# Kernel tuning notes

Hardware: AMD Instinct MI355X
Metric: run time of the kernel (lower is better)

The kernel has to match this reference:

```python
import jax, jax.numpy as jnp
import numpy as np

# Irreps structure (hardcoded per init_kwargs):
#  input  = 16x0e + 8x1o  -> dim 16 + 8*3 = 40
#  query  = key = 8x0e + 4x1o -> dim 8 + 4*3 = 20
#  output = 16x0e + 8x1o -> dim 40
#  edge_sh = 1x0e + 1x1o -> dim 4
M0, M1 = 16, 8          # input multiplicities (scalar, vector)
Q0, Q1 = 8, 4           # query/key multiplicities
O0, O1 = 16, 8          # output multiplicities
TPK_NUMEL = M0*Q0 + M1*Q0 + M0*Q1 + M1*Q1 + M1*Q1   # 320
TPV_NUMEL = M0*O0 + M1*O0 + M0*O1 + M1*O1 + M1*O1   # 640
EDGE_BASIS = 16
HIDDEN = 32


def _split(x):
    """Split irreps vector [*, m0 + 3*m1] into scalars [*, m0] and vectors [*, m1, 3]."""
    m0 = x.shape[-1] - 3 * ((x.shape[-1] - M0) // 3) if False else None
    return x  # placeholder, not used


def fc_net(x, w1, w2):
    """e3nn FullyConnectedNet: no biases, 1/sqrt(fan_in) scaling, silu hidden act."""
    h = jax.nn.silu((x @ w1) * (1.0 / np.sqrt(x.shape[-1])))
    return (h @ w2) * (1.0 / np.sqrt(w1.shape[-1]))


def fctp_edge(xs, xv, shs, shv, w, o0, o1):
    """FullyConnectedTensorProduct((m0x0e+m1x1o) x (1x0e+1x1o) -> (o0x0e+o1x1o))
    with per-edge weights w [E, numel]. Component-normalized CG, path-normalized output.
    xs:[E,m0] xv:[E,m1,3] shs:[E,1] shv:[E,3]."""
    m0, m1 = xs.shape[1], xv.shape[1]
    sizes = [m0*o0, m1*o0, m0*o1, m1*o1, m1*o1]
    offs = np.cumsum([0] + sizes)
    w1 = w[:, offs[0]:offs[1]].reshape(-1, m0, o0)
    w2 = w[:, offs[1]:offs[2]].reshape(-1, m1, o0)
    w3 = w[:, offs[2]:offs[3]].reshape(-1, m0, o1)
    w4 = w[:, offs[3]:offs[4]].reshape(-1, m1, o1)
    w5 = w[:, offs[4]:offs[5]].reshape(-1, m1, o1)
    # scalar output paths: 0e x 0e -> 0e ; 1o x 1o -> 0e (dot / sqrt3)
    p_ss = xs * shs                                            # [E,m0]
    p_vv = jnp.einsum('eic,ec->ei', xv, shv) * (1.0/np.sqrt(3.0))  # [E,m1]
    out_s = (jnp.einsum('ei,eio->eo', p_ss, w1)
             + jnp.einsum('ei,eio->eo', p_vv, w2)) * (1.0/np.sqrt(m0 + m1))
    # vector output paths: 0e x 1o ; 1o x 0e ; 1o x 1o -> 1o (cross / sqrt2)
    p_sv = xs[:, :, None] * shv[:, None, :]                    # [E,m0,3]
    p_vs = xv * shs[:, :, None]                                # [E,m1,3]
    p_xx = jnp.cross(xv, shv[:, None, :]) * (1.0/np.sqrt(2.0)) # [E,m1,3]
    out_v = (jnp.einsum('eic,eio->eoc', p_sv, w3)
             + jnp.einsum('eic,eio->eoc', p_vs, w4)
             + jnp.einsum('eic,eio->eoc', p_xx, w5)) * (1.0/np.sqrt(m0 + 2*m1))
    return out_s, out_v


def setup_inputs() -> dict:
    key = jax.random.key(0)
    ks = jax.random.split(key, 12)
    N, E = 10000, 100000
    node_ft = jax.random.normal(ks[0], (N, M0 + 3*M1), dtype=jnp.float32)
    edge_index = jax.random.randint(ks[1], (2, E), 0, N, dtype=jnp.int64)
    edge_sh = jax.random.normal(ks[2], (E, 4), dtype=jnp.float32)
    edge_scalars = jax.random.uniform(ks[3], (E, EDGE_BASIS), dtype=jnp.float32)
    # learned parameters
    w_q_s = jax.random.normal(ks[4], (M0, Q0), dtype=jnp.float32)
    w_q_v = jax.random.normal(ks[5], (M1, Q1), dtype=jnp.float32)
    fck_w1 = jax.random.normal(ks[6], (EDGE_BASIS, HIDDEN), dtype=jnp.float32)
    fck_w2 = jax.random.normal(ks[7], (HIDDEN, TPK_NUMEL), dtype=jnp.float32)
    fcv_w1 = jax.random.normal(ks[8], (EDGE_BASIS, HIDDEN), dtype=jnp.float32)
    fcv_w2 = jax.random.normal(ks[9], (HIDDEN, TPV_NUMEL), dtype=jnp.float32)
    wdot_s = jax.random.normal(ks[10], (Q0, Q0), dtype=jnp.float32)
    wdot_v = jax.random.normal(ks[11], (Q1, Q1), dtype=jnp.float32)
    return dict(node_ft=node_ft, edge_index=edge_index, edge_sh=edge_sh,
                edge_scalars=edge_scalars, w_q_s=w_q_s, w_q_v=w_q_v,
                fck_w1=fck_w1, fck_w2=fck_w2, fcv_w1=fcv_w1, fcv_w2=fcv_w2,
                wdot_s=wdot_s, wdot_v=wdot_v)


def reference(node_ft, edge_index, edge_sh, edge_scalars, w_q_s, w_q_v,
              fck_w1, fck_w2, fcv_w1, fcv_w2, wdot_s, wdot_v):
    N = node_ft.shape[0]
    sender, receiver = edge_index[0], edge_index[1]
    x_s = node_ft[:, :M0]                       # [N,16]
    x_v = node_ft[:, M0:].reshape(N, M1, 3)     # [N,8,3]
    # q = o3.Linear(input -> query): per-irrep linear mixing, 1/sqrt(mul) norm
    q_s = (x_s @ w_q_s) * (1.0/np.sqrt(M0))                    # [N,Q0]
    q_v = jnp.einsum('nic,io->noc', x_v, w_q_v) * (1.0/np.sqrt(M1))  # [N,Q1,3]
    sh_s, sh_v = edge_sh[:, :1], edge_sh[:, 1:4]
    xs_e, xv_e = x_s[sender], x_v[sender]       # gather sender features
    # per-edge tensor-product weights from radial MLPs
    wk = fc_net(edge_scalars, fck_w1, fck_w2)   # [E, 320]
    wv = fc_net(edge_scalars, fcv_w1, fcv_w2)   # [E, 640]
    k_s, k_v = fctp_edge(xs_e, xv_e, sh_s, sh_v, wk, Q0, Q1)
    v_s, v_v = fctp_edge(xs_e, xv_e, sh_s, sh_v, wv, O0, O1)
    # dot = FCTP(query, key -> 0e) with shared internal weights
    qr_s, qr_v = q_s[receiver], q_v[receiver]
    fan = Q0*Q0 + Q1*Q1
    dot = (jnp.einsum('ei,ej,ij->e', qr_s, k_s, wdot_s)
           + jnp.einsum('eic,ejc,ij->e', qr_v, k_v, wdot_v) * (1.0/np.sqrt(3.0))
           ) * (1.0/np.sqrt(fan))               # [E]
    # scatter-softmax over receiver
    ex = jnp.exp(dot)
    z = jax.ops.segment_sum(ex, receiver, num_segments=N)      # [N]
    alpha = ex / z[receiver]
    a = jnp.sqrt(jax.nn.relu(alpha))            # [E]
    out_s = jax.ops.segment_sum(a[:, None] * v_s, receiver, num_segments=N)
    out_v = jax.ops.segment_sum(a[:, None, None] * v_v, receiver, num_segments=N)
    return jnp.concatenate([out_s, out_v.reshape(N, O1*3)], axis=-1)  # [N,40]
```

## Files before the change

### kernel.cpp

```cpp
#include <hip/hip_runtime.h>


#define BS 256
#define EPB 64

typedef _Float16 h2 __attribute__((ext_vector_type(2)));

__device__ __forceinline__ float silu_f(float x) {
    return x * (1.0f / (1.0f + __expf(-x)));
}
__device__ __forceinline__ unsigned short f2h(float f) {
    return __builtin_bit_cast(unsigned short, (_Float16)f);
}
__device__ __forceinline__ unsigned pk2h(float a, float b) {
    return (unsigned)f2h(a) | ((unsigned)f2h(b) << 16);
}
__device__ __forceinline__ h2 uh2(unsigned u) {
    return __builtin_bit_cast(h2, u);
}
__device__ __forceinline__ h2 pkrtz(float a, float b) {
    return __builtin_bit_cast(h2, __builtin_amdgcn_cvt_pkrtz(a, b));
}
__device__ __forceinline__ h2 pfma(h2 a, h2 b, h2 c) {
    return __builtin_elementwise_fma(a, b, c);
}
__device__ __forceinline__ float h2s(h2 a) {
    return (float)a[0] + (float)a[1];
}
__device__ __forceinline__ float wred4(float v) {
    v += __shfl_xor(v, 16);
    v += __shfl_xor(v, 32);
    return v;
}

__global__ __launch_bounds__(256) void pre_count(
    const float* __restrict__ node_ft,
    const int*   __restrict__ ei,
    const float* __restrict__ w_q_s, const float* __restrict__ w_q_v,
    const float* __restrict__ wdot_s, const float* __restrict__ wdot_v,
    float* __restrict__ qd, int* __restrict__ cnt, int* __restrict__ flag,
    int N, int E)
{
    const int gid = blockIdx.x * blockDim.x + threadIdx.x;

    int acc = 0;
    if ((threadIdx.x & 63) == 0) {
        const int kmax = (E < 64) ? E : 64;
        for (int k = 0; k < kmax; ++k) acc |= ei[2*k + 1];
    }
    acc = __shfl(acc, 0, 64);
    const int is64 = (acc == 0) ? 1 : 0;
    if (gid == 0) *flag = is64;

    if (gid < E) {
        const int rcv = is64 ? ei[2*(E + gid)] : ei[E + gid];
        atomicAdd(cnt + rcv, 1);
    }

    const int n = gid;
    if (n >= N) return;

    const float* nf = node_ft + (size_t)n * 40;
    float xs[16];
#pragma unroll
    for (int i = 0; i < 16; ++i) xs[i] = nf[i];
    float qv0[8];
#pragma unroll
    for (int o = 0; o < 8; ++o) {
        float a = 0.f;
#pragma unroll
        for (int i = 0; i < 16; ++i) a += xs[i] * w_q_s[i*8 + o];
        qv0[o] = a * 0.25f;
    }
    float* qdn = qd + (size_t)n * 20;
#pragma unroll
    for (int j = 0; j < 8; ++j) {
        float a = 0.f;
#pragma unroll
        for (int i = 0; i < 8; ++i) a += qv0[i] * wdot_s[i*8 + j];
        qdn[j] = a;
    }
    float xv[8][3];
#pragma unroll
    for (int i = 0; i < 8; ++i)
#pragma unroll
        for (int c = 0; c < 3; ++c) xv[i][c] = nf[16 + i*3 + c];
    float qv[4][3];
#pragma unroll
    for (int o = 0; o < 4; ++o)
#pragma unroll
        for (int c = 0; c < 3; ++c) {
            float a = 0.f;
#pragma unroll
            for (int i = 0; i < 8; ++i) a += xv[i][c] * w_q_v[i*4 + o];
            qv[o][c] = a * 0.35355339059327379f;
        }
#pragma unroll
    for (int j = 0; j < 4; ++j)
#pragma unroll
        for (int c = 0; c < 3; ++c) {
            float a = 0.f;
#pragma unroll
            for (int i = 0; i < 4; ++i) a += qv[i][c] * wdot_v[i*4 + j];
            qdn[8 + j*3 + c] = a;
        }
}

__global__ __launch_bounds__(1024) void scan_kernel(
    const int* __restrict__ cnt, int* __restrict__ start,
    int* __restrict__ cursor, int N)
{
    __shared__ int wsum[16];
    __shared__ int s_carry;
    const int tid = threadIdx.x, wave = tid >> 6, lane = tid & 63;
    if (tid == 0) s_carry = 0;
    __syncthreads();
    for (int base = 0; base < N; base += 1024) {
        const int i = base + tid;
        const int v = (i < N) ? cnt[i] : 0;
        int x = v;
#pragma unroll
        for (int d = 1; d < 64; d <<= 1) {
            const int y = __shfl_up(x, d, 64);
            if (lane >= d) x += y;
        }
        if (lane == 63) wsum[wave] = x;
        __syncthreads();
        if (wave == 0 && lane < 16) {
            int w = wsum[lane];
#pragma unroll
            for (int d = 1; d < 16; d <<= 1) {
                const int y = __shfl_up(w, d, 64);
                if (lane >= d) w += y;
            }
            wsum[lane] = w;
        }
        __syncthreads();
        const int woff = (wave == 0) ? 0 : wsum[wave - 1];
        const int carry = s_carry;
        if (i < N) {
            const int s = carry + woff + x - v;
            start[i] = s;
            cursor[i] = s;
        }
        __syncthreads();
        if (tid == 0) s_carry = carry + wsum[15];
        __syncthreads();
    }
    if (tid == 0) start[N] = s_carry;
}

__global__ __launch_bounds__(BS) void edge_all(
    const float* __restrict__ node_ft,
    const int*   __restrict__ ei,
    const float* __restrict__ edge_sh,
    const float* __restrict__ edge_scalars,
    const float* __restrict__ fck_w1,
    const float* __restrict__ fck_w2,
    const float* __restrict__ fcv_w1,
    const float* __restrict__ fcv_w2,
    const float* __restrict__ qd,
    int*   __restrict__ cursor,
    float* __restrict__ exbuf,
    float* __restrict__ vbuf,
    const int* __restrict__ flag,
    int N, int E)
{
    __shared__ uint4 swz[4 * 385];

    const int tid = threadIdx.x;
    const int lane = tid & 63;
    const int p = lane >> 4;
    const int q = lane & 15;
    const int w = tid >> 6;
    const int e = blockIdx.x * EPB + w * 16 + q;
    const bool val = (e < E);
    const int ec = val ? e : (E - 1);

    const int is64 = *flag;
    const int snd = is64 ? ei[2*ec]       : ei[ec];
    const int rcv = is64 ? ei[2*(E + ec)] : ei[E + ec];

    int pos = 0;
    if (p == 0 && val) pos = atomicAdd(cursor + rcv, 1);

    const float4 s4 = *(const float4*)(edge_sh + (size_t)ec * 4);
    const float sh_s = s4.x;
    const float sh_v[3] = {s4.y, s4.z, s4.w};
    const float* nf = node_ft + (size_t)snd * 40;
    const float c3 = 0.57735026918962576f;
    const float c7 = 0.70710678118654752f;

    float es[16];
    {
        const float4* a0 = (const float4*)(edge_scalars + (size_t)ec * 16);
#pragma unroll
        for (int t = 0; t < 4; ++t) {
            const float4 v = a0[t];
            es[4*t+0]=v.x; es[4*t+1]=v.y; es[4*t+2]=v.z; es[4*t+3]=v.w;
        }
    }

    for (int idx = tid; idx < 4 * 320; idx += BS) {
        const int pg = idx / 320;
        const int local = idx - pg * 320;
        unsigned r0, r1, r2, r3;
        if (local < 128) {
            const int j = local >> 2, rr = local & 3, ip = rr >> 1, h = rr & 1;
            const int i0 = 4*pg + 2*ip;
            const float* s0 = fck_w2 + j*320 + i0*8 + 4*h;
            const float* s1 = s0 + 8;
            r0 = pk2h(s0[0], s1[0]); r1 = pk2h(s0[1], s1[1]);
            r2 = pk2h(s0[2], s1[2]); r3 = pk2h(s0[3], s1[3]);
        } else if (local < 192) {
            const int l = local - 128; const int j = l >> 1, ip = l & 1;
            const int i0 = 4*pg + 2*ip;
            const float* s0 = fck_w2 + j*320 + 192 + i0*4;
            const float* s1 = s0 + 4;
            r0 = pk2h(s0[0], s1[0]); r1 = pk2h(s0[1], s1[1]);
            r2 = pk2h(s0[2], s1[2]); r3 = pk2h(s0[3], s1[3]);
        } else if (local < 256) {
            const int l = local - 192; const int j = l >> 1, h = l & 1;
            const int i0 = 2*pg;
            const float* s0 = fck_w2 + j*320 + 128 + i0*8 + 4*h;
            const float* s1 = s0 + 8;
            r0 = pk2h(s0[0], s1[0]); r1 = pk2h(s0[1], s1[1]);
            r2 = pk2h(s0[2], s1[2]); r3 = pk2h(s0[3], s1[3]);
        } else {
            const int l = local - 256; const int jp = l >> 2, rr = l & 3;
            const int il = rr >> 1, h = rr & 1;
            const int i = 2*pg + il, j0 = 2*jp;
            const int col = (h == 0 ? 256 : 288) + i*4;
            const float* s0 = fck_w2 + j0*320 + col;
            const float* s1 = s0 + 320;
            r0 = pk2h(s0[0], s1[0]); r1 = pk2h(s0[1], s1[1]);
            r2 = pk2h(s0[2], s1[2]); r3 = pk2h(s0[3], s1[3]);
        }
        swz[pg * 321 + local] = make_uint4(r0, r1, r2, r3);
    }
    __syncthreads();

    float sa = 0.f;
    {
        float hk[32];
#pragma unroll
        for (int j = 0; j < 32; ++j) {
            float a = 0.f;
#pragma unroll
            for (int t = 0; t < 16; ++t) a += es[t] * fck_w1[t*32 + j];
            hk[j] = silu_f(a * 0.25f);
        }

        const uint4* g = swz + p * 321;

        const h2 xs01 = pkrtz(nf[4*p + 0], nf[4*p + 1]);
        const h2 xs23 = pkrtz(nf[4*p + 2], nf[4*p + 3]);
        const float x00 = nf[16 + 6*p], x01 = nf[17 + 6*p], x02 = nf[18 + 6*p];
        const float x10 = nf[19 + 6*p], x11 = nf[20 + 6*p], x12 = nf[21 + 6*p];
        const h2 pvp = pkrtz((x00*sh_v[0] + x01*sh_v[1] + x02*sh_v[2]) * c3,
                             (x10*sh_v[0] + x11*sh_v[1] + x12*sh_v[2]) * c3);

        h2 K1[8] = {}, K3[4] = {}, K2[8] = {};
#pragma unroll
        for (int j = 0; j < 32; ++j) {
            const uint4 A = g[j*4+0], B = g[j*4+1], C = g[j*4+2], D = g[j*4+3];
            const uint4 Ea = g[128 + j*2], Fb = g[128 + j*2 + 1];
            const uint4 U = g[192 + j*2], V = g[192 + j*2 + 1];
            const h2 hh = pkrtz(hk[j], hk[j]);
            const h2 t01 = hh * xs01, t23 = hh * xs23, tp = hh * pvp;
            K1[0]=pfma(t01,uh2(A.x),K1[0]); K1[0]=pfma(t23,uh2(C.x),K1[0]);
            K1[1]=pfma(t01,uh2(A.y),K1[1]); K1[1]=pfma(t23,uh2(C.y),K1[1]);
            K1[2]=pfma(t01,uh2(A.z),K1[2]); K1[2]=pfma(t23,uh2(C.z),K1[2]);
            K1[3]=pfma(t01,uh2(A.w),K1[3]); K1[3]=pfma(t23,uh2(C.w),K1[3]);
            K1[4]=pfma(t01,uh2(B.x),K1[4]); K1[4]=pfma(t23,uh2(D.x),K1[4]);
            K1[5]=pfma(t01,uh2(B.y),K1[5]); K1[5]=pfma(t23,uh2(D.y),K1[5]);
            K1[6]=pfma(t01,uh2(B.z),K1[6]); K1[6]=pfma(t23,uh2(D.z),K1[6]);
            K1[7]=pfma(t01,uh2(B.w),K1[7]); K1[7]=pfma(t23,uh2(D.w),K1[7]);
            K3[0]=pfma(t01,uh2(Ea.x),K3[0]); K3[0]=pfma(t23,uh2(Fb.x),K3[0]);
            K3[1]=pfma(t01,uh2(Ea.y),K3[1]); K3[1]=pfma(t23,uh2(Fb.y),K3[1]);
            K3[2]=pfma(t01,uh2(Ea.z),K3[2]); K3[2]=pfma(t23,uh2(Fb.z),K3[2]);
            K3[3]=pfma(t01,uh2(Ea.w),K3[3]); K3[3]=pfma(t23,uh2(Fb.w),K3[3]);
            K2[0]=pfma(tp,uh2(U.x),K2[0]); K2[1]=pfma(tp,uh2(U.y),K2[1]);
            K2[2]=pfma(tp,uh2(U.z),K2[2]); K2[3]=pfma(tp,uh2(U.w),K2[3]);
            K2[4]=pfma(tp,uh2(V.x),K2[4]); K2[5]=pfma(tp,uh2(V.y),K2[5]);
            K2[6]=pfma(tp,uh2(V.z),K2[6]); K2[7]=pfma(tp,uh2(V.w),K2[7]);
        }

        h2 P4[8] = {}, P5[8] = {};
#pragma unroll
        for (int jp = 0; jp < 16; ++jp) {
            const uint4 a4 = g[256 + jp*4 + 0];
            const uint4 b4 = g[256 + jp*4 + 1];
            const uint4 c4 = g[256 + jp*4 + 2];
            const uint4 d4 = g[256 + jp*4 + 3];
            const h2 hp = pkrtz(hk[2*jp], hk[2*jp+1]);
            P4[0]=pfma(hp,uh2(a4.x),P4[0]); P4[1]=pfma(hp,uh2(a4.y),P4[1]);
            P4[2]=pfma(hp,uh2(a4.z),P4[2]); P4[3]=pfma(hp,uh2(a4.w),P4[3]);
            P5[0]=pfma(hp,uh2(b4.x),P5[0]); P5[1]=pfma(hp,uh2(b4.y),P5[1]);
            P5[2]=pfma(hp,uh2(b4.z),P5[2]); P5[3]=pfma(hp,uh2(b4.w),P5[3]);
            P4[4]=pfma(hp,uh2(c4.x),P4[4]); P4[5]=pfma(hp,uh2(c4.y),P4[5]);
            P4[6]=pfma(hp,uh2(c4.z),P4[6]); P4[7]=pfma(hp,uh2(c4.w),P4[7]);
            P5[4]=pfma(hp,uh2(d4.x),P5[4]); P5[5]=pfma(hp,uh2(d4.y),P5[5]);
            P5[6]=pfma(hp,uh2(d4.z),P5[6]); P5[7]=pfma(hp,uh2(d4.w),P5[7]);
        }

        float ds = 0.f, dv = 0.f;
        {
            float qdr[20];
            const float4* rp = (const float4*)(qd + (size_t)rcv * 20);
#pragma unroll
            for (int t = 0; t < 5; ++t) {
                const float4 a = rp[t];
                qdr[4*t+0]=a.x; qdr[4*t+1]=a.y; qdr[4*t+2]=a.z; qdr[4*t+3]=a.w;
            }
#pragma unroll
            for (int o = 0; o < 8; ++o)
                ds += qdr[o] * (sh_s*h2s(K1[o]) + h2s(K2[o]));
            float KV[12] = {};
            {
                const float s0=sh_s*x00, s1=sh_s*x01, s2=sh_s*x02;
                const float cx0=c7*(x01*sh_v[2]-x02*sh_v[1]);
                const float cx1=c7*(x02*sh_v[0]-x00*sh_v[2]);
                const float cx2=c7*(x00*sh_v[1]-x01*sh_v[0]);
#pragma unroll
                for (int o = 0; o < 4; ++o) {
                    const float w4 = h2s(P4[o]), w5 = h2s(P5[o]);
                    KV[o*3+0] += s0*w4 + cx0*w5;
                    KV[o*3+1] += s1*w4 + cx1*w5;
                    KV[o*3+2] += s2*w4 + cx2*w5;
                }
            }
            {
                const float s0=sh_s*x10, s1=sh_s*x11, s2=sh_s*x12;
                const float cx0=c7*(x11*sh_v[2]-x12*sh_v[1]);
                const float cx1=c7*(x12*sh_v[0]-x10*sh_v[2]);
                const float cx2=c7*(x10*sh_v[1]-x11*sh_v[0]);
#pragma unroll
                for (int o = 0; o < 4; ++o) {
                    const float w4 = h2s(P4[4+o]), w5 = h2s(P5[4+o]);
                    KV[o*3+0] += s0*w4 + cx0*w5;
                    KV[o*3+1] += s1*w4 + cx1*w5;
                    KV[o*3+2] += s2*w4 + cx2*w5;
                }
            }
#pragma unroll
            for (int o = 0; o < 4; ++o) {
                const float k3 = h2s(K3[o]);
#pragma unroll
                for (int c = 0; c < 3; ++c)
                    dv += qdr[8 + o*3 + c] * (k3*sh_v[c] + KV[o*3+c]);
            }
        }
        ds = wred4(ds); dv = wred4(dv);

        if (p == 0 && val) {
            const float dot = ds * 4.0343567508008e-3f + dv * 2.0171788261497e-3f;
            sa = __expf(0.5f * dot);
            exbuf[pos] = sa * sa;
        }
    }

    __syncthreads();
    for (int idx = tid; idx < 4 * 384; idx += BS) {
        const int pg = idx / 384;
        const int local = idx - pg * 384;
        const float* s0;
        const float* s1;
        if (local < 256) {
            const int j = local >> 3, rr = local & 7, ip = rr >> 2, h = rr & 3;
            const int i0 = 4*pg + 2*ip;
            s0 = fcv_w2 + j*640 + i0*16 + h*4;
            s1 = s0 + 16;
        } else {
            const int l = local - 256; const int j = l >> 2, h = l & 3;
            const int i0 = 2*pg;
            s0 = fcv_w2 + j*640 + 256 + i0*16 + h*4;
            s1 = s0 + 16;
        }
        swz[pg * 385 + local] = make_uint4(
            pk2h(s0[0], s1[0]), pk2h(s0[1], s1[1]),
            pk2h(s0[2], s1[2]), pk2h(s0[3], s1[3]));
    }
    __syncthreads();

    float hv[32];
#pragma unroll
    for (int j = 0; j < 32; ++j) {
        float a = 0.f;
#pragma unroll
        for (int t = 0; t < 16; ++t) a += es[t] * fcv_w1[t*32 + j];
        hv[j] = silu_f(a * 0.25f);
    }

    {
        const uint4* g = swz + p * 385;

        const h2 xs01 = pkrtz(nf[4*p + 0]*sh_s, nf[4*p + 1]*sh_s);
        const h2 xs23 = pkrtz(nf[4*p + 2]*sh_s, nf[4*p + 3]*sh_s);
        const h2 pvp = pkrtz(
            (nf[16+6*p]*sh_v[0] + nf[17+6*p]*sh_v[1] + nf[18+6*p]*sh_v[2]) * c3,
            (nf[19+6*p]*sh_v[0] + nf[20+6*p]*sh_v[1] + nf[21+6*p]*sh_v[2]) * c3);

        h2 Aa[16] = {};
#pragma unroll
        for (int j = 0; j < 32; ++j) {
            const uint4* gw = g + j*8;
            const uint4 a0 = gw[0], a1 = gw[1], a2 = gw[2], a3 = gw[3];
            const uint4 b0 = gw[4], b1 = gw[5], b2 = gw[6], b3 = gw[7];
            const uint4* g2 = g + 256 + j*4;
            const uint4 u0 = g2[0], u1 = g2[1], u2 = g2[2], u3 = g2[3];
            const h2 hh = pkrtz(hv[j], hv[j]);
            const h2 t01 = hh * xs01, t23 = hh * xs23, tp = hh * pvp;
            Aa[0] =pfma(t01,uh2(a0.x),Aa[0]);  Aa[0] =pfma(t23,uh2(b0.x),Aa[0]);  Aa[0] =pfma(tp,uh2(u0.x),Aa[0]);
            Aa[1] =pfma(t01,uh2(a0.y),Aa[1]);  Aa[1] =pfma(t23,uh2(b0.y),Aa[1]);  Aa[1] =pfma(tp,uh2(u0.y),Aa[1]);
            Aa[2] =pfma(t01,uh2(a0.z),Aa[2]);  Aa[2] =pfma(t23,uh2(b0.z),Aa[2]);  Aa[2] =pfma(tp,uh2(u0.z),Aa[2]);
            Aa[3] =pfma(t01,uh2(a0.w),Aa[3]);  Aa[3] =pfma(t23,uh2(b0.w),Aa[3]);  Aa[3] =pfma(tp,uh2(u0.w),Aa[3]);
            Aa[4] =pfma(t01,uh2(a1.x),Aa[4]);  Aa[4] =pfma(t23,uh2(b1.x),Aa[4]);  Aa[4] =pfma(tp,uh2(u1.x),Aa[4]);
            Aa[5] =pfma(t01,uh2(a1.y),Aa[5]);  Aa[5] =pfma(t23,uh2(b1.y),Aa[5]);  Aa[5] =pfma(tp,uh2(u1.y),Aa[5]);
            Aa[6] =pfma(t01,uh2(a1.z),Aa[6]);  Aa[6] =pfma(t23,uh2(b1.z),Aa[6]);  Aa[6] =pfma(tp,uh2(u1.z),Aa[6]);
            Aa[7] =pfma(t01,uh2(a1.w),Aa[7]);  Aa[7] =pfma(t23,uh2(b1.w),Aa[7]);  Aa[7] =pfma(tp,uh2(u1.w),Aa[7]);
            Aa[8] =pfma(t01,uh2(a2.x),Aa[8]);  Aa[8] =pfma(t23,uh2(b2.x),Aa[8]);  Aa[8] =pfma(tp,uh2(u2.x),Aa[8]);
            Aa[9] =pfma(t01,uh2(a2.y),Aa[9]);  Aa[9] =pfma(t23,uh2(b2.y),Aa[9]);  Aa[9] =pfma(tp,uh2(u2.y),Aa[9]);
            Aa[10]=pfma(t01,uh2(a2.z),Aa[10]); Aa[10]=pfma(t23,uh2(b2.z),Aa[10]); Aa[10]=pfma(tp,uh2(u2.z),Aa[10]);
            Aa[11]=pfma(t01,uh2(a2.w),Aa[11]); Aa[11]=pfma(t23,uh2(b2.w),Aa[11]); Aa[11]=pfma(tp,uh2(u2.w),Aa[11]);
            Aa[12]=pfma(t01,uh2(a3.x),Aa[12]); Aa[12]=pfma(t23,uh2(b3.x),Aa[12]); Aa[12]=pfma(tp,uh2(u3.x),Aa[12]);
            Aa[13]=pfma(t01,uh2(a3.y),Aa[13]); Aa[13]=pfma(t23,uh2(b3.y),Aa[13]); Aa[13]=pfma(tp,uh2(u3.y),Aa[13]);
            Aa[14]=pfma(t01,uh2(a3.z),Aa[14]); Aa[14]=pfma(t23,uh2(b3.z),Aa[14]); Aa[14]=pfma(tp,uh2(u3.z),Aa[14]);
            Aa[15]=pfma(t01,uh2(a3.w),Aa[15]); Aa[15]=pfma(t23,uh2(b3.w),Aa[15]); Aa[15]=pfma(tp,uh2(u3.w),Aa[15]);
        }

        float A0[16];
#pragma unroll
        for (int o = 0; o < 16; ++o) A0[o] = wred4(h2s(Aa[o]));

        if (p == 0 && val) {
            const float cs = 0.03608439182435161f;
            float4* vp = (float4*)(vbuf + (size_t)pos * 40);
#pragma unroll
            for (int t = 0; t < 4; ++t) {
                float4 r;
                r.x = sa * A0[4*t+0] * cs; r.y = sa * A0[4*t+1] * cs;
                r.z = sa * A0[4*t+2] * cs; r.w = sa * A0[4*t+3] * cs;
                vp[t] = r;
            }
        }
    }

    __syncthreads();
    for (int idx = tid; idx < 4 * 256; idx += BS) {
        const int pg = idx >> 8;
        const int local = idx & 255;
        const float* s0;
        const float* s1;
        if (local < 128) {
            const int j = local >> 2, rr = local & 3, ip = rr >> 1, h = rr & 1;
            const int i0 = 4*pg + 2*ip;
            s0 = fcv_w2 + j*640 + 384 + i0*8 + 4*h;
            s1 = s0 + 8;
        } else {
            const int l = local - 128;
            const int jp = l >> 3, rr = l & 7, il = rr >> 2, h2c = rr & 3;
            const int i = 2*pg + il, j0 = 2*jp;
            const int base = (h2c < 2) ? 512 : 576;
            s0 = fcv_w2 + j0*640 + base + i*8 + (h2c & 1)*4;
            s1 = s0 + 640;
        }
        swz[pg * 257 + local] = make_uint4(
            pk2h(s0[0], s1[0]), pk2h(s0[1], s1[1]),
            pk2h(s0[2], s1[2]), pk2h(s0[3], s1[3]));
    }
    __syncthreads();

    {
        const uint4* g = swz + p * 257;

        const h2 xs01 = pkrtz(nf[4*p + 0], nf[4*p + 1]);
        const h2 xs23 = pkrtz(nf[4*p + 2], nf[4*p + 3]);

        h2 T3[8] = {};
#pragma unroll
        for (int j = 0; j < 32; ++j) {
            const uint4 E0 = g[j*4+0], E1 = g[j*4+1];
            const uint4 F0 = g[j*4+2], F1 = g[j*4+3];
            const h2 hh = pkrtz(hv[j], hv[j]);
            const h2 t01 = hh * xs01, t23 = hh * xs23;
            T3[0]=pfma(t01,uh2(E0.x),T3[0]); T3[0]=pfma(t23,uh2(F0.x),T3[0]);
            T3[1]=pfma(t01,uh2(E0.y),T3[1]); T3[1]=pfma(t23,uh2(F0.y),T3[1]);
            T3[2]=pfma(t01,uh2(E0.z),T3[2]); T3[2]=pfma(t23,uh2(F0.z),T3[2]);
            T3[3]=pfma(t01,uh2(E0.w),T3[3]); T3[3]=pfma(t23,uh2(F0.w),T3[3]);
            T3[4]=pfma(t01,uh2(E1.x),T3[4]); T3[4]=pfma(t23,uh2(F1.x),T3[4]);
            T3[5]=pfma(t01,uh2(E1.y),T3[5]); T3[5]=pfma(t23,uh2(F1.y),T3[5]);
            T3[6]=pfma(t01,uh2(E1.z),T3[6]); T3[6]=pfma(t23,uh2(F1.z),T3[6]);
            T3[7]=pfma(t01,uh2(E1.w),T3[7]); T3[7]=pfma(t23,uh2(F1.w),T3[7]);
        }

        h2 P4[16] = {}, P5[16] = {};
#pragma unroll
        for (int jp = 0; jp < 16; ++jp) {
            const uint4* gw = g + 128 + jp*8;
            const uint4 a4 = gw[0], b4 = gw[1];
            const uint4 c4 = gw[2], d4 = gw[3];
            const uint4 e4 = gw[4], f4 = gw[5];
            const uint4 m4 = gw[6], n4 = gw[7];
            const h2 hp = pkrtz(hv[2*jp], hv[2*jp+1]);
            P4[0] =pfma(hp,uh2(a4.x),P4[0]);  P4[1] =pfma(hp,uh2(a4.y),P4[1]);
            P4[2] =pfma(hp,uh2(a4.z),P4[2]);  P4[3] =pfma(hp,uh2(a4.w),P4[3]);
            P4[4] =pfma(hp,uh2(b4.x),P4[4]);  P4[5] =pfma(hp,uh2(b4.y),P4[5]);
            P4[6] =pfma(hp,uh2(b4.z),P4[6]);  P4[7] =pfma(hp,uh2(b4.w),P4[7]);
            P5[0] =pfma(hp,uh2(c4.x),P5[0]);  P5[1] =pfma(hp,uh2(c4.y),P5[1]);
            P5[2] =pfma(hp,uh2(c4.z),P5[2]);  P5[3] =pfma(hp,uh2(c4.w),P5[3]);
            P5[4] =pfma(hp,uh2(d4.x),P5[4]);  P5[5] =pfma(hp,uh2(d4.y),P5[5]);
            P5[6] =pfma(hp,uh2(d4.z),P5[6]);  P5[7] =pfma(hp,uh2(d4.w),P5[7]);
            P4[8] =pfma(hp,uh2(e4.x),P4[8]);  P4[9] =pfma(hp,uh2(e4.y),P4[9]);
            P4[10]=pfma(hp,uh2(e4.z),P4[10]); P4[11]=pfma(hp,uh2(e4.w),P4[11]);
            P4[12]=pfma(hp,uh2(f4.x),P4[12]); P4[13]=pfma(hp,uh2(f4.y),P4[13]);
            P4[14]=pfma(hp,uh2(f4.z),P4[14]); P4[15]=pfma(hp,uh2(f4.w),P4[15]);
            P5[8] =pfma(hp,uh2(m4.x),P5[8]);  P5[9] =pfma(hp,uh2(m4.y),P5[9]);
            P5[10]=pfma(hp,uh2(m4.z),P5[10]); P5[11]=pfma(hp,uh2(m4.w),P5[11]);
            P5[12]=pfma(hp,uh2(n4.x),P5[12]); P5[13]=pfma(hp,uh2(n4.y),P5[13]);
            P5[14]=pfma(hp,uh2(n4.z),P5[14]); P5[15]=pfma(hp,uh2(n4.w),P5[15]);
        }

        float R[24], T3f[8];
        {
            float acc[24];
#pragma unroll
            for (int o = 0; o < 24; ++o) acc[o] = 0.f;
            {
                const float x0 = nf[16 + 6*p], x1 = nf[17 + 6*p], x2 = nf[18 + 6*p];
                const float s0 = sh_s*x0, s1 = sh_s*x1, s2 = sh_s*x2;
                const float cx0 = c7*(x1*sh_v[2] - x2*sh_v[1]);
                const float cx1 = c7*(x2*sh_v[0] - x0*sh_v[2]);
                const float cx2 = c7*(x0*sh_v[1] - x1*sh_v[0]);
#pragma unroll
                for (int o = 0; o < 8; ++o) {
                    const float w4 = h2s(P4[o]), w5 = h2s(P5[o]);
                    acc[o*3+0] += s0*w4 + cx0*w5;
                    acc[o*3+1] += s1*w4 + cx1*w5;
                    acc[o*3+2] += s2*w4 + cx2*w5;
                }
            }
            {
                const float x0 = nf[19 + 6*p], x1 = nf[20 + 6*p], x2 = nf[21 + 6*p];
                const float s0 = sh_s*x0, s1 = sh_s*x1, s2 = sh_s*x2;
                const float cx0 = c7*(x1*sh_v[2] - x2*sh_v[1]);
                const float cx1 = c7*(x2*sh_v[0] - x0*sh_v[2]);
                const float cx2 = c7*(x0*sh_v[1] - x1*sh_v[0]);
#pragma unroll
                for (int o = 0; o < 8; ++o) {
                    const float w4 = h2s(P4[8+o]), w5 = h2s(P5[8+o]);
                    acc[o*3+0] += s0*w4 + cx0*w5;
                    acc[o*3+1] += s1*w4 + cx1*w5;
                    acc[o*3+2] += s2*w4 + cx2*w5;
                }
            }
#pragma unroll
            for (int o = 0; o < 24; ++o) R[o] = wred4(acc[o]);
        }
#pragma unroll
        for (int o = 0; o < 8; ++o) T3f[o] = wred4(h2s(T3[o]));

        if (p == 0 && val) {
            const float sc = 0.03125f;
            float row[24];
#pragma unroll
            for (int o = 0; o < 8; ++o)
#pragma unroll
                for (int c = 0; c < 3; ++c)
                    row[o*3+c] = sa * (T3f[o]*sh_v[c] + R[o*3+c]) * sc;
            float4* vp = (float4*)(vbuf + (size_t)pos * 40 + 16);
#pragma unroll
            for (int t = 0; t < 6; ++t) {
                float4 r; r.x = row[4*t+0]; r.y = row[4*t+1]; r.z = row[4*t+2]; r.w = row[4*t+3];
                vp[t] = r;
            }
        }
    }
}

__global__ __launch_bounds__(256) void node_reduce(
    const int*   __restrict__ start,
    const float* __restrict__ exbuf,
    const float* __restrict__ vbuf,
    float* __restrict__ out, int N)
{
    const int wave = threadIdx.x >> 6;
    const int lane = threadIdx.x & 63;
    const int n = blockIdx.x * 4 + wave;
    if (n >= N) return;
    const int r0 = start[n], r1 = start[n + 1];
    float z = 0.f, comp = 0.f;
    for (int r = r0; r < r1; ++r) {
        z += exbuf[r];
        if (lane < 40) comp += vbuf[(size_t)r * 40 + lane];
    }
    if (lane < 40)
        out[(size_t)n * 40 + lane] = (z > 0.f) ? comp * rsqrtf(z) : 0.f;
}

extern "C" void kernel_launch(void* const* d_in, const int* in_sizes, int n_in,
                              void* d_out, int out_size, void* d_ws, size_t ws_size,
                              hipStream_t stream) {
    const float* node_ft      = (const float*)d_in[0];
    const int*   edge_index   = (const int*)  d_in[1];
    const float* edge_sh      = (const float*)d_in[2];
    const float* edge_scalars = (const float*)d_in[3];
    const float* w_q_s        = (const float*)d_in[4];
    const float* w_q_v        = (const float*)d_in[5];
    const float* fck_w1       = (const float*)d_in[6];
    const float* fck_w2       = (const float*)d_in[7];
    const float* fcv_w1       = (const float*)d_in[8];
    const float* fcv_w2       = (const float*)d_in[9];
    const float* wdot_s       = (const float*)d_in[10];
    const float* wdot_v       = (const float*)d_in[11];

    const int N = in_sizes[0] / 40;
    const int E = in_sizes[2] / 4;

    float* ws    = (float*)d_ws;
    float* qd    = ws;
    int*   cnt   = (int*)(ws + (size_t)N * 20);
    int*   start = cnt + N;
    int*   curs  = start + N + 1;
    int*   flg   = curs + N;
    size_t off   = (size_t)N * 20 + N + (N + 1) + N + 1;
    off = (off + 3) & ~(size_t)3;
    float* exbuf  = ws + off;
    float* vbuf   = exbuf + E;

    float* out = (float*)d_out;

    const int NE = (E > N) ? E : N;
    const int EB = (E + EPB - 1) / EPB;

    hipMemsetAsync(cnt, 0, (size_t)N * sizeof(int), stream);
    hipLaunchKernelGGL(pre_count, dim3((NE + 255) / 256), dim3(256), 0, stream,
                       node_ft, edge_index, w_q_s, w_q_v, wdot_s, wdot_v,
                       qd, cnt, flg, N, E);
    hipLaunchKernelGGL(scan_kernel, dim3(1), dim3(1024), 0, stream,
                       cnt, start, curs, N);
    hipLaunchKernelGGL(edge_all, dim3(EB), dim3(BS), 0, stream,
                       node_ft, edge_index, edge_sh, edge_scalars,
                       fck_w1, fck_w2, fcv_w1, fcv_w2,
                       qd, curs, exbuf, vbuf, flg, N, E);
    hipLaunchKernelGGL(node_reduce, dim3((N + 3) / 4), dim3(256), 0, stream,
                       start, exbuf, vbuf, out, N);
}
```

Measured before the change: 241.7 us.

## Prepack fp16 swizzled weights once in pre-pass and interleave exp into vbuf rows

The fp32 to fp16 packing and swizzling of fck_w2/fcv_w2 now happens once in pre_count and is written to a workspace buffer. Each edge_all block then copies the prepacked uint4s into shared memory instead of recomputing them. The hidden-layer MLP compute is moved ahead of the barrier so it overlaps the LDS fill, and the softmax exponent is stored as column 40 of a 44-wide vbuf row, so node_reduce reads one array. The cost is a wider vbuf row and extra work in pre_count, which assumes the grid covers at least 3840 threads.

```diff
diff --git a/kernel.cpp b/kernel.cpp
--- a/kernel.cpp
+++ b/kernel.cpp
@@ -38,7 +38,9 @@
     const int*   __restrict__ ei,
     const float* __restrict__ w_q_s, const float* __restrict__ w_q_v,
     const float* __restrict__ wdot_s, const float* __restrict__ wdot_v,
+    const float* __restrict__ fck_w2, const float* __restrict__ fcv_w2,
     float* __restrict__ qd, int* __restrict__ cnt, int* __restrict__ flag,
+    uint4* __restrict__ pk,
     int N, int E)
 {
     const int gid = blockIdx.x * blockDim.x + threadIdx.x;
@@ -55,6 +57,86 @@
     if (gid < E) {
         const int rcv = is64 ? ei[2*(E + gid)] : ei[E + gid];
         atomicAdd(cnt + rcv, 1);
+    }
+
+    if (gid < 3840) {
+        uint4 r;
+        if (gid < 1280) {
+            const int pg = gid / 320;
+            const int local = gid - pg * 320;
+            if (local < 128) {
+                const int j = local >> 2, rr = local & 3, ip = rr >> 1, h = rr & 1;
+                const int i0 = 4*pg + 2*ip;
+                const float* s0 = fck_w2 + j*320 + i0*8 + 4*h;
+                const float* s1 = s0 + 8;
+                r = make_uint4(pk2h(s0[0], s1[0]), pk2h(s0[1], s1[1]),
+                               pk2h(s0[2], s1[2]), pk2h(s0[3], s1[3]));
+            } else if (local < 192) {
+                const int l = local - 128; const int j = l >> 1, ip = l & 1;
+                const int i0 = 4*pg + 2*ip;
+                const float* s0 = fck_w2 + j*320 + 192 + i0*4;
+                const float* s1 = s0 + 4;
+                r = make_uint4(pk2h(s0[0], s1[0]), pk2h(s0[1], s1[1]),
+                               pk2h(s0[2], s1[2]), pk2h(s0[3], s1[3]));
+            } else if (local < 256) {
+                const int l = local - 192; const int j = l >> 1, h = l & 1;
+                const int i0 = 2*pg;
+                const float* s0 = fck_w2 + j*320 + 128 + i0*8 + 4*h;
+                const float* s1 = s0 + 8;
+                r = make_uint4(pk2h(s0[0], s1[0]), pk2h(s0[1], s1[1]),
+                               pk2h(s0[2], s1[2]), pk2h(s0[3], s1[3]));
+            } else {
+                const int l = local - 256; const int jp = l >> 2, rr = l & 3;
+                const int il = rr >> 1, h = rr & 1;
+                const int i = 2*pg + il, j0 = 2*jp;
+                const int col = (h == 0 ? 256 : 288) + i*4;
+                const float* s0 = fck_w2 + j0*320 + col;
+                const float* s1 = s0 + 320;
+                r = make_uint4(pk2h(s0[0], s1[0]), pk2h(s0[1], s1[1]),
+                               pk2h(s0[2], s1[2]), pk2h(s0[3], s1[3]));
+            }
+        } else if (gid < 2816) {
+            const int l2 = gid - 1280;
+            const int pg = l2 / 384;
+            const int local = l2 - pg * 384;
+            const float* s0;
+            const float* s1;
+            if (local < 256) {
+                const int j = local >> 3, rr = local & 7, ip = rr >> 2, h = rr & 3;
+                const int i0 = 4*pg + 2*ip;
+                s0 = fcv_w2 + j*640 + i0*16 + h*4;
+                s1 = s0 + 16;
+            } else {
+                const int l = local - 256; const int j = l >> 2, h = l & 3;
+                const int i0 = 2*pg;
+                s0 = fcv_w2 + j*640 + 256 + i0*16 + h*4;
+                s1 = s0 + 16;
+            }
+            r = make_uint4(pk2h(s0[0], s1[0]), pk2h(s0[1], s1[1]),
+                           pk2h(s0[2], s1[2]), pk2h(s0[3], s1[3]));
+        } else {
+            const int l2 = gid - 2816;
+            const int pg = l2 >> 8;
+            const int local = l2 & 255;
+            const float* s0;
+            const float* s1;
+            if (local < 128) {
+                const int j = local >> 2, rr = local & 3, ip = rr >> 1, h = rr & 1;
+                const int i0 = 4*pg + 2*ip;
+                s0 = fcv_w2 + j*640 + 384 + i0*8 + 4*h;
+                s1 = s0 + 8;
+            } else {
+                const int l = local - 128;
+                const int jp = l >> 3, rr = l & 7, il = rr >> 2, h2c = rr & 3;
+                const int i = 2*pg + il, j0 = 2*jp;
+                const int base = (h2c < 2) ? 512 : 576;
+                s0 = fcv_w2 + j0*640 + base + i*8 + (h2c & 1)*4;
+                s1 = s0 + 640;
+            }
+            r = make_uint4(pk2h(s0[0], s1[0]), pk2h(s0[1], s1[1]),
+                           pk2h(s0[2], s1[2]), pk2h(s0[3], s1[3]));
+        }
+        pk[gid] = r;
     }
 
     const int n = gid;
@@ -156,12 +238,10 @@
     const float* __restrict__ edge_sh,
     const float* __restrict__ edge_scalars,
     const float* __restrict__ fck_w1,
-    const float* __restrict__ fck_w2,
     const float* __restrict__ fcv_w1,
-    const float* __restrict__ fcv_w2,
+    const uint4* __restrict__ pk,
     const float* __restrict__ qd,
     int*   __restrict__ cursor,
-    float* __restrict__ exbuf,
     float* __restrict__ vbuf,
     const int* __restrict__ flag,
     int N, int E)
@@ -201,56 +281,25 @@
         }
     }
 
-    for (int idx = tid; idx < 4 * 320; idx += BS) {
+#pragma unroll
+    for (int it = 0; it < 5; ++it) {
+        const int idx = it * BS + tid;
         const int pg = idx / 320;
-        const int local = idx - pg * 320;
-        unsigned r0, r1, r2, r3;
-        if (local < 128) {
-            const int j = local >> 2, rr = local & 3, ip = rr >> 1, h = rr & 1;
-            const int i0 = 4*pg + 2*ip;
-            const float* s0 = fck_w2 + j*320 + i0*8 + 4*h;
-            const float* s1 = s0 + 8;
-            r0 = pk2h(s0[0], s1[0]); r1 = pk2h(s0[1], s1[1]);
-            r2 = pk2h(s0[2], s1[2]); r3 = pk2h(s0[3], s1[3]);
-        } else if (local < 192) {
-            const int l = local - 128; const int j = l >> 1, ip = l & 1;
-            const int i0 = 4*pg + 2*ip;
-            const float* s0 = fck_w2 + j*320 + 192 + i0*4;
-            const float* s1 = s0 + 4;
-            r0 = pk2h(s0[0], s1[0]); r1 = pk2h(s0[1], s1[1]);
-            r2 = pk2h(s0[2], s1[2]); r3 = pk2h(s0[3], s1[3]);
-        } else if (local < 256) {
-            const int l = local - 192; const int j = l >> 1, h = l & 1;
-            const int i0 = 2*pg;
-            const float* s0 = fck_w2 + j*320 + 128 + i0*8 + 4*h;
-            const float* s1 = s0 + 8;
-            r0 = pk2h(s0[0], s1[0]); r1 = pk2h(s0[1], s1[1]);
-            r2 = pk2h(s0[2], s1[2]); r3 = pk2h(s0[3], s1[3]);
-        } else {
-            const int l = local - 256; const int jp = l >> 2, rr = l & 3;
-            const int il = rr >> 1, h = rr & 1;
-            const int i = 2*pg + il, j0 = 2*jp;
-            const int col = (h == 0 ? 256 : 288) + i*4;
-            const float* s0 = fck_w2 + j0*320 + col;
-            const float* s1 = s0 + 320;
-            r0 = pk2h(s0[0], s1[0]); r1 = pk2h(s0[1], s1[1]);
-            r2 = pk2h(s0[2], s1[2]); r3 = pk2h(s0[3], s1[3]);
-        }
-        swz[pg * 321 + local] = make_uint4(r0, r1, r2, r3);
+        swz[pg * 321 + (idx - pg * 320)] = pk[idx];
+    }
+
+    float sa = 0.f;
+    float hk[32];
+#pragma unroll
+    for (int j = 0; j < 32; ++j) {
+        float a = 0.f;
+#pragma unroll
+        for (int t = 0; t < 16; ++t) a += es[t] * fck_w1[t*32 + j];
+        hk[j] = silu_f(a * 0.25f);
     }
     __syncthreads();
 
-    float sa = 0.f;
     {
-        float hk[32];
-#pragma unroll
-        for (int j = 0; j < 32; ++j) {
-            float a = 0.f;
-#pragma unroll
-            for (int t = 0; t < 16; ++t) a += es[t] * fck_w1[t*32 + j];
-            hk[j] = silu_f(a * 0.25f);
-        }
-
         const uint4* g = swz + p * 321;
 
         const h2 xs01 = pkrtz(nf[4*p + 0], nf[4*p + 1]);
@@ -356,32 +405,17 @@
         if (p == 0 && val) {
             const float dot = ds * 4.0343567508008e-3f + dv * 2.0171788261497e-3f;
             sa = __expf(0.5f * dot);
-            exbuf[pos] = sa * sa;
+            vbuf[(size_t)pos * 44 + 40] = sa * sa;
         }
     }
 
     __syncthreads();
-    for (int idx = tid; idx < 4 * 384; idx += BS) {
+#pragma unroll
+    for (int it = 0; it < 6; ++it) {
+        const int idx = it * BS + tid;
         const int pg = idx / 384;
-        const int local = idx - pg * 384;
-        const float* s0;
-        const float* s1;
-        if (local < 256) {
-            const int j = local >> 3, rr = local & 7, ip = rr >> 2, h = rr & 3;
-            const int i0 = 4*pg + 2*ip;
-            s0 = fcv_w2 + j*640 + i0*16 + h*4;
-            s1 = s0 + 16;
-        } else {
-            const int l = local - 256; const int j = l >> 2, h = l & 3;
-            const int i0 = 2*pg;
-            s0 = fcv_w2 + j*640 + 256 + i0*16 + h*4;
-            s1 = s0 + 16;
-        }
-        swz[pg * 385 + local] = make_uint4(
-            pk2h(s0[0], s1[0]), pk2h(s0[1], s1[1]),
-            pk2h(s0[2], s1[2]), pk2h(s0[3], s1[3]));
-    }
-    __syncthreads();
+        swz[pg * 385 + (idx - pg * 384)] = pk[1280 + idx];
+    }
 
     float hv[32];
 #pragma unroll
@@ -391,6 +425,7 @@
         for (int t = 0; t < 16; ++t) a += es[t] * fcv_w1[t*32 + j];
         hv[j] = silu_f(a * 0.25f);
     }
+    __syncthreads();
 
     {
         const uint4* g = swz + p * 385;
@@ -435,7 +470,7 @@
 
         if (p == 0 && val) {
             const float cs = 0.03608439182435161f;
-            float4* vp = (float4*)(vbuf + (size_t)pos * 40);
+            float4* vp = (float4*)(vbuf + (size_t)pos * 44);
 #pragma unroll
             for (int t = 0; t < 4; ++t) {
                 float4 r;
@@ -447,27 +482,11 @@
     }
 
     __syncthreads();
-    for (int idx = tid; idx < 4 * 256; idx += BS) {
+#pragma unroll
+    for (int it = 0; it < 4; ++it) {
+        const int idx = it * BS + tid;
         const int pg = idx >> 8;
-        const int local = idx & 255;
-        const float* s0;
-        const float* s1;
-        if (local < 128) {
-            const int j = local >> 2, rr = local & 3, ip = rr >> 1, h = rr & 1;
-            const int i0 = 4*pg + 2*ip;
-            s0 = fcv_w2 + j*640 + 384 + i0*8 + 4*h;
-            s1 = s0 + 8;
-        } else {
-            const int l = local - 128;
-            const int jp = l >> 3, rr = l & 7, il = rr >> 2, h2c = rr & 3;
-            const int i = 2*pg + il, j0 = 2*jp;
-            const int base = (h2c < 2) ? 512 : 576;
-            s0 = fcv_w2 + j0*640 + base + i*8 + (h2c & 1)*4;
-            s1 = s0 + 640;
-        }
-        swz[pg * 257 + local] = make_uint4(
-            pk2h(s0[0], s1[0]), pk2h(s0[1], s1[1]),
-            pk2h(s0[2], s1[2]), pk2h(s0[3], s1[3]));
+        swz[pg * 257 + (idx & 255)] = pk[2816 + idx];
     }
     __syncthreads();
 
@@ -568,7 +587,7 @@
 #pragma unroll
                 for (int c = 0; c < 3; ++c)
                     row[o*3+c] = sa * (T3f[o]*sh_v[c] + R[o*3+c]) * sc;
-            float4* vp = (float4*)(vbuf + (size_t)pos * 40 + 16);
+            float4* vp = (float4*)(vbuf + (size_t)pos * 44 + 16);
 #pragma unroll
             for (int t = 0; t < 6; ++t) {
                 float4 r; r.x = row[4*t+0]; r.y = row[4*t+1]; r.z = row[4*t+2]; r.w = row[4*t+3];
@@ -580,7 +599,6 @@
 
 __global__ __launch_bounds__(256) void node_reduce(
     const int*   __restrict__ start,
-    const float* __restrict__ exbuf,
     const float* __restrict__ vbuf,
     float* __restrict__ out, int N)
 {
@@ -591,8 +609,9 @@
     const int r0 = start[n], r1 = start[n + 1];
     float z = 0.f, comp = 0.f;
     for (int r = r0; r < r1; ++r) {
-        z += exbuf[r];
-        if (lane < 40) comp += vbuf[(size_t)r * 40 + lane];
+        const float* row = vbuf + (size_t)r * 44;
+        z += row[40];
+        if (lane < 40) comp += row[lane];
     }
     if (lane < 40)
         out[(size_t)n * 40 + lane] = (z > 0.f) ? comp * rsqrtf(z) : 0.f;
@@ -625,8 +644,8 @@
     int*   flg   = curs + N;
     size_t off   = (size_t)N * 20 + N + (N + 1) + N + 1;
     off = (off + 3) & ~(size_t)3;
-    float* exbuf  = ws + off;
-    float* vbuf   = exbuf + E;
+    uint4* pk    = (uint4*)(ws + off);
+    float* vbuf  = ws + off + 15360;
 
     float* out = (float*)d_out;
 
@@ -636,13 +655,12 @@
     hipMemsetAsync(cnt, 0, (size_t)N * sizeof(int), stream);
     hipLaunchKernelGGL(pre_count, dim3((NE + 255) / 256), dim3(256), 0, stream,
                        node_ft, edge_index, w_q_s, w_q_v, wdot_s, wdot_v,
-                       qd, cnt, flg, N, E);
+                       fck_w2, fcv_w2, qd, cnt, flg, pk, N, E);
     hipLaunchKernelGGL(scan_kernel, dim3(1), dim3(1024), 0, stream,
                        cnt, start, curs, N);
     hipLaunchKernelGGL(edge_all, dim3(EB), dim3(BS), 0, stream,
                        node_ft, edge_index, edge_sh, edge_scalars,
-                       fck_w1, fck_w2, fcv_w1, fcv_w2,
-                       qd, curs, exbuf, vbuf, flg, N, E);
+                       fck_w1, fcv_w1, pk, qd, curs, vbuf, flg, N, E);
     hipLaunchKernelGGL(node_reduce, dim3((N + 3) / 4), dim3(256), 0, stream,
-                       start, exbuf, vbuf, out, N);
-}
+                       start, vbuf, out, N);
+}
```

New measurement: 240.8 us, median of 2. Within noise of the previous version (-0.4%).
